# Optimization experiments

Hardware: AMD Instinct MI355X
Metric: run time of the kernel (lower is better)

## Reference

```python
import jax, jax.numpy as jnp
import numpy as np

N_NODES = 100000
N_EDGES = 1600000
IN_CH = 128
HID = 64
N_CLASSES = 16
N_GRAPHS = 64


def setup_inputs() -> dict:
    key = jax.random.key(0)
    ks = jax.random.split(key, 10)
    x = jax.random.normal(ks[0], (N_NODES, IN_CH), dtype=jnp.float32)
    edge_index = jax.random.randint(ks[1], (2, N_EDGES), 0, N_NODES, dtype=jnp.int64)
    edge_weight = jax.random.uniform(ks[2], (N_EDGES,), dtype=jnp.float32)
    batch = jnp.sort(jax.random.randint(ks[3], (N_NODES,), 0, N_GRAPHS, dtype=jnp.int64))
    s1 = 1.0 / np.sqrt(IN_CH)
    s2 = 1.0 / np.sqrt(HID)
    W1 = jax.random.uniform(ks[4], (IN_CH, HID), jnp.float32, -s1, s1)
    b1 = jnp.zeros((HID,), jnp.float32)
    W2 = jax.random.uniform(ks[5], (HID, HID), jnp.float32, -s2, s2)
    b2 = jnp.zeros((HID,), jnp.float32)
    Wl = jax.random.uniform(ks[6], (HID, N_CLASSES), jnp.float32, -s2, s2)
    bl = jax.random.uniform(ks[7], (N_CLASSES,), jnp.float32, -s2, s2)
    return {"x": x, "edge_index": edge_index, "edge_weight": edge_weight,
            "batch": batch, "W1": W1, "b1": b1, "W2": W2, "b2": b2,
            "Wl": Wl, "bl": bl}


def _gcn_conv(x, src, dst, ew, W, b, n_nodes):
    # PyG GCNConv: h = x @ W; symmetric normalization with self-loops;
    # out[dst] += norm * h[src]; out += bias.
    deg = jax.ops.segment_sum(ew, dst, num_segments=n_nodes)
    deg_inv_sqrt = jnp.where(deg > 0, jax.lax.rsqrt(jnp.maximum(deg, 1e-30)), 0.0)
    norm = deg_inv_sqrt[src] * ew * deg_inv_sqrt[dst]  # [E']
    h = x @ W                                          # [N, out]
    msg = h[src] * norm[:, None]                       # [E', out] gather
    out = jax.ops.segment_sum(msg, dst, num_segments=n_nodes)  # scatter-add
    return out + b


def reference(x, edge_index, edge_weight, batch, W1, b1, W2, b2, Wl, bl):
    n = x.shape[0]
    # add self loops once (weight 1.0), shared by both conv layers
    loop = jnp.arange(n, dtype=edge_index.dtype)
    src = jnp.concatenate([edge_index[0], loop])
    dst = jnp.concatenate([edge_index[1], loop])
    ew = jnp.concatenate([edge_weight, jnp.ones((n,), edge_weight.dtype)])

    h = jax.nn.relu(_gcn_conv(x, src, dst, ew, W1, b1, n))
    h = jax.nn.relu(_gcn_conv(h, src, dst, ew, W2, b2, n))

    # global_mean_pool over graphs
    sums = jax.ops.segment_sum(h, batch, num_segments=N_GRAPHS)  # [G, HID]
    cnt = jax.ops.segment_sum(jnp.ones((n,), h.dtype), batch, num_segments=N_GRAPHS)
    pooled = sums / jnp.maximum(cnt, 1.0)[:, None]

    return pooled @ Wl + bl
```

## Files before the change

### kernel.cpp

```cpp
#include <hip/hip_runtime.h>
#include <hip/hip_fp16.h>

#define N_NODES   100000
#define N_EDGES   1600000
#define IN_CH     128
#define HID       64
#define N_CLASSES 16
#define N_GRAPHS  64

#define BK_SH     9
#define BK_NODES  512
#define NB        ((N_NODES + BK_NODES - 1) / BK_NODES)
#define BK_CAP    10240
#define CH_EDGES  4096
#define EPT       16
#define NCH       ((N_EDGES + CH_EDGES - 1) / CH_EDGES)
#define AGG_NPW   2

typedef __attribute__((ext_vector_type(8))) short bf16x8;
typedef __attribute__((ext_vector_type(4))) float f32x4;
typedef __attribute__((ext_vector_type(4))) unsigned u32x4;
typedef __attribute__((ext_vector_type(2))) unsigned u32x2;

__device__ __forceinline__ unsigned short f2bf(float f) {
    unsigned u = __float_as_uint(f);
    u += 0x7fffu + ((u >> 16) & 1u);
    return (unsigned short)(u >> 16);
}
__device__ __forceinline__ f32x4 bf4v(uint2 v) {
    u32x4 u;
    u.x = v.x << 16; u.y = v.x & 0xffff0000u;
    u.z = v.y << 16; u.w = v.y & 0xffff0000u;
    return __builtin_bit_cast(f32x4, u);
}
__device__ __forceinline__ float dec_ew(unsigned v) {
    return __half2float(__ushort_as_half((unsigned short)(v >> 17)));
}

#if __has_builtin(__builtin_amdgcn_make_buffer_rsrc) && \
    __has_builtin(__builtin_amdgcn_raw_buffer_load_b32) && \
    __has_builtin(__builtin_amdgcn_raw_buffer_load_b64)
struct BufView {
    __amdgpu_buffer_rsrc_t rsrc;
    __device__ __forceinline__ void init(const void* p) {
        rsrc = __builtin_amdgcn_make_buffer_rsrc((void*)p, (short)0,
                                                 (int)0xFFFFFFFF, 0x00020000);
    }
    __device__ __forceinline__ unsigned ld32(unsigned off) const {
        return __builtin_amdgcn_raw_buffer_load_b32(rsrc, (int)off, 0, 0);
    }
    __device__ __forceinline__ uint2 ld64(unsigned off) const {
        u32x2 r = __builtin_amdgcn_raw_buffer_load_b64(rsrc, (int)off, 0, 0);
        return make_uint2(r.x, r.y);
    }
};
#else
struct BufView {
    const char* base;
    __device__ __forceinline__ void init(const void* p) { base = (const char*)p; }
    __device__ __forceinline__ unsigned ld32(unsigned off) const {
        return *(const unsigned*)(base + off);
    }
    __device__ __forceinline__ uint2 ld64(unsigned off) const {
        return *(const uint2*)(base + off);
    }
};
#endif

__global__ void k_init(int* __restrict__ bcursor, float* __restrict__ pooled,
                       float* __restrict__ cnt) {
    int i = blockIdx.x * 256 + threadIdx.x;
    if (i < NB) bcursor[i] = i * BK_CAP;
    if (i < N_GRAPHS * HID) pooled[i] = 0.0f;
    if (i < N_GRAPHS) cnt[i] = 0.0f;
}

__global__ void k_binscatter(const int* __restrict__ src, const int* __restrict__ dst,
                             const float* __restrict__ ew, int* __restrict__ bcursor,
                             int2* __restrict__ bedges) {
    __shared__ int  hist[NB];
    __shared__ int  offs[NB];
    __shared__ int  gbase[NB];
    __shared__ int  sc[256];
    __shared__ int2 stage[CH_EDGES];
    __shared__ int  dest[CH_EDGES];
    const int t = threadIdx.x;
    const int base = blockIdx.x * CH_EDGES;
    const int nloc = min(CH_EDGES, N_EDGES - base);

    for (int i = t; i < NB; i += 256) hist[i] = 0;
    __syncthreads();

    int myb[EPT], myr[EPT], myp[EPT]; float myw[EPT];
#pragma unroll
    for (int j = 0; j < EPT; ++j) {
        int i = base + j * 256 + t;
        if (i < N_EDGES) {
            int s = src[i], d = dst[i];
            int b = d >> BK_SH;
            myb[j] = b;
            myr[j] = atomicAdd(&hist[b], 1);
            myp[j] = s | ((d & (BK_NODES - 1)) << 17);
            myw[j] = ew[i];
        } else {
            myb[j] = -1;
        }
    }
    __syncthreads();

    int v = (t < NB) ? hist[t] : 0;
    sc[t] = v;
    __syncthreads();
    for (int off = 1; off < 256; off <<= 1) {
        int a = (t >= off) ? sc[t - off] : 0;
        __syncthreads();
        sc[t] += a;
        __syncthreads();
    }
    if (t < NB) {
        offs[t] = sc[t] - v;
        gbase[t] = (v > 0) ? atomicAdd(&bcursor[t], v) : 0;
    }
    __syncthreads();

#pragma unroll
    for (int j = 0; j < EPT; ++j) {
        if (myb[j] >= 0) {
            int p = offs[myb[j]] + myr[j];
            stage[p] = make_int2(myp[j], __float_as_int(myw[j]));
            dest[p] = gbase[myb[j]] + myr[j];
        }
    }
    __syncthreads();

    for (int i = t; i < nloc; i += 256)
        bedges[dest[i]] = stage[i];
}

__global__ __launch_bounds__(256) void k_build(const int* __restrict__ bcursor,
                                               const int2* __restrict__ bedges,
                                               int2* __restrict__ rowse,
                                               float* __restrict__ dis,
                                               unsigned* __restrict__ csr) {
    __shared__ int2  eds[BK_CAP];
    __shared__ int   cnt[BK_NODES];
    __shared__ float dsum[BK_NODES];
    __shared__ int   cur[BK_NODES];
    __shared__ int   sc[256];
    const int b = blockIdx.x;
    const int t = threadIdx.x;
    const int beg = b * BK_CAP, end = bcursor[b];
    const int n = end - beg;

    for (int i = t; i < BK_NODES; i += 256) { cnt[i] = 0; dsum[i] = 0.0f; }
    __syncthreads();

    for (int i = t; i < n; i += 256) {
        int2 e = bedges[beg + i];
        eds[i] = e;
        int dl = ((unsigned)e.x) >> 17;
        atomicAdd(&cnt[dl], 1);
        atomicAdd(&dsum[dl], __int_as_float(e.y));
    }
    __syncthreads();

    int a0 = cnt[2 * t], a1 = cnt[2 * t + 1];
    int pair = a0 + a1;
    sc[t] = pair;
    __syncthreads();
    for (int off = 1; off < 256; off <<= 1) {
        int a = (t >= off) ? sc[t - off] : 0;
        __syncthreads();
        sc[t] += a;
        __syncthreads();
    }
    int excl = sc[t] - pair;
    cur[2 * t] = excl;
    cur[2 * t + 1] = excl + a0;
    {
        int n0 = b * BK_NODES + 2 * t;
        if (n0 < N_NODES) {
            rowse[n0] = make_int2(beg + excl, beg + excl + a0);
            dis[n0] = rsqrtf(1.0f + dsum[2 * t]);
        }
        int n1 = n0 + 1;
        if (n1 < N_NODES) {
            rowse[n1] = make_int2(beg + excl + a0, beg + excl + a0 + a1);
            dis[n1] = rsqrtf(1.0f + dsum[2 * t + 1]);
        }
    }
    __syncthreads();

    for (int i = t; i < n; i += 256) {
        int2 e = eds[i];
        int dl = ((unsigned)e.x) >> 17;
        int s = e.x & 0x1FFFF;
        unsigned short w16 = __half_as_ushort(__float2half(__int_as_float(e.y)));
        int pos = beg + atomicAdd(&cur[dl], 1);
        csr[pos] = (unsigned)s | ((unsigned)w16 << 17);
    }
}

template <int K, bool INB>
__global__ __launch_bounds__(256) void k_gemm(const float* __restrict__ x,
                                              const unsigned short* __restrict__ xb,
                                              const float* __restrict__ W,
                                              const float* __restrict__ dis,
                                              unsigned short* __restrict__ hb) {
    constexpr int AS = K + 8;
    __shared__ unsigned short wt[64 * AS];
    const int t    = threadIdx.x;
    const int lane = t & 63;
    const int wave = t >> 6;
    const int m    = lane & 15;
    const int quad = lane >> 4;
    const int rowbase = blockIdx.x * 64;

    bf16x8 afrag[K / 32];

    if constexpr (!INB) {
        __shared__ unsigned short a_s[64 * AS];
        constexpr int CPR = K / 8;
        for (int c = t; c < 64 * CPR; c += 256) {
            int row = c / CPR, cc = c % CPR;
            int gr = rowbase + row;
            float4 v0, v1;
            if (gr < N_NODES) {
                v0 = *(const float4*)&x[(long)gr * K + cc * 8];
                v1 = *(const float4*)&x[(long)gr * K + cc * 8 + 4];
            } else {
                v0 = make_float4(0.f, 0.f, 0.f, 0.f); v1 = v0;
            }
            uint4 p;
            p.x = f2bf(v0.x) | ((unsigned)f2bf(v0.y) << 16);
            p.y = f2bf(v0.z) | ((unsigned)f2bf(v0.w) << 16);
            p.z = f2bf(v1.x) | ((unsigned)f2bf(v1.y) << 16);
            p.w = f2bf(v1.z) | ((unsigned)f2bf(v1.w) << 16);
            *(uint4*)&a_s[row * AS + cc * 8] = p;
        }
        for (int idx = t; idx < K * 64; idx += 256) {
            int k = idx >> 6, n = idx & 63;
            wt[n * AS + k] = f2bf(W[idx]);
        }
        __syncthreads();
#pragma unroll
        for (int ks = 0; ks < K / 32; ++ks)
            afrag[ks] = *(const bf16x8*)&a_s[(wave * 16 + m) * AS + ks * 32 + quad * 8];
    } else {
        const int gr = rowbase + wave * 16 + m;
#pragma unroll
        for (int ks = 0; ks < K / 32; ++ks) {
            if (gr < N_NODES)
                afrag[ks] = *(const bf16x8*)&xb[(long)gr * K + ks * 32 + quad * 8];
            else
                afrag[ks] = (bf16x8){0, 0, 0, 0, 0, 0, 0, 0};
        }
        for (int idx = t; idx < K * 64; idx += 256) {
            int k = idx >> 6, n = idx & 63;
            wt[n * AS + k] = f2bf(W[idx]);
        }
        __syncthreads();
    }

    bf16x8 bfrag[4][K / 32];
#pragma unroll
    for (int nt = 0; nt < 4; ++nt)
#pragma unroll
        for (int ks = 0; ks < K / 32; ++ks)
            bfrag[nt][ks] = *(const bf16x8*)&wt[(nt * 16 + m) * AS + ks * 32 + quad * 8];

    f32x4 acc[4];
#pragma unroll
    for (int nt = 0; nt < 4; ++nt) acc[nt] = (f32x4){0.f, 0.f, 0.f, 0.f};

#pragma unroll
    for (int ks = 0; ks < K / 32; ++ks) {
#pragma unroll
        for (int nt = 0; nt < 4; ++nt)
            acc[nt] = __builtin_amdgcn_mfma_f32_16x16x32_bf16(afrag[ks], bfrag[nt][ks],
                                                              acc[nt], 0, 0, 0);
    }

#pragma unroll
    for (int i = 0; i < 4; ++i) {
        int gr = rowbase + wave * 16 + quad * 4 + i;
        if (gr < N_NODES) {
            float dsc = dis[gr];
#pragma unroll
            for (int nt = 0; nt < 4; ++nt)
                hb[(long)gr * HID + nt * 16 + m] = f2bf(dsc * acc[nt][i]);
        }
    }
}

template <bool OB>
__global__ void k_aggregate(const int2* __restrict__ rowse, const unsigned* __restrict__ csr,
                            const uint2* __restrict__ hb, const float* __restrict__ dis,
                            const float* __restrict__ b, float4* __restrict__ out4,
                            uint2* __restrict__ outb) {
    const int tid  = threadIdx.x;
    const int lane = tid & 63;
    const int g    = lane >> 4;
    const int c4   = lane & 15;
    const int nodebase = (blockIdx.x * 4 + (tid >> 6)) * AGG_NPW;
    const float4 bb = ((const float4*)b)[c4];
    const f32x4 bbv = {bb.x, bb.y, bb.z, bb.w};

    if (nodebase >= N_NODES) return;

    BufView vc; vc.init(csr);
    BufView vh; vh.init(hb);
    const unsigned coff = (unsigned)(c4 << 3);

    int2 rs = rowse[nodebase];
    uint2 hsr = hb[nodebase * 16 + c4];

    for (int j = 0; j < AGG_NPW; ++j) {
        const int node = nodebase + j;
        const int2 rs_c = rs;
        const f32x4 hsv = bf4v(hsr);
        if (j + 1 < AGG_NPW) {
            rs  = rowse[node + 1];
            hsr = hb[(node + 1) * 16 + c4];
        }

        f32x4 acc = (g == 0) ? hsv : (f32x4){0.f, 0.f, 0.f, 0.f};

        int p = rs_c.x;
        const int end = rs_c.y;

        unsigned d0, d1, d2, d3;
        if (p + 16 <= end) {
            const unsigned v = (unsigned)((p + g) << 2);
            d0 = vc.ld32(v);      d1 = vc.ld32(v + 16);
            d2 = vc.ld32(v + 32); d3 = vc.ld32(v + 48);
        }
        while (p + 16 <= end) {
            const unsigned e0 = d0, e1 = d1, e2 = d2, e3 = d3;
            const int pn = p + 16;
            if (pn + 16 <= end) {
                const unsigned v = (unsigned)((pn + g) << 2);
                d0 = vc.ld32(v);      d1 = vc.ld32(v + 16);
                d2 = vc.ld32(v + 32); d3 = vc.ld32(v + 48);
            }
            f32x4 v0 = bf4v(vh.ld64(((e0 & 0x1FFFF) << 7) | coff));
            f32x4 v1 = bf4v(vh.ld64(((e1 & 0x1FFFF) << 7) | coff));
            f32x4 v2 = bf4v(vh.ld64(((e2 & 0x1FFFF) << 7) | coff));
            f32x4 v3 = bf4v(vh.ld64(((e3 & 0x1FFFF) << 7) | coff));
            acc += v0 * dec_ew(e0);
            acc += v1 * dec_ew(e1);
            acc += v2 * dec_ew(e2);
            acc += v3 * dec_ew(e3);
            p = pn;
        }
        if (p < end) {
            const int i0 = p + g, i1 = p + 4 + g, i2 = p + 8 + g, i3 = p + 12 + g;
            const int last = end - 1;
            unsigned e0 = vc.ld32((unsigned)(min(i0, last) << 2));
            unsigned e1 = vc.ld32((unsigned)(min(i1, last) << 2));
            unsigned e2 = vc.ld32((unsigned)(min(i2, last) << 2));
            unsigned e3 = vc.ld32((unsigned)(min(i3, last) << 2));
            f32x4 v0 = bf4v(vh.ld64(((e0 & 0x1FFFF) << 7) | coff));
            f32x4 v1 = bf4v(vh.ld64(((e1 & 0x1FFFF) << 7) | coff));
            f32x4 v2 = bf4v(vh.ld64(((e2 & 0x1FFFF) << 7) | coff));
            f32x4 v3 = bf4v(vh.ld64(((e3 & 0x1FFFF) << 7) | coff));
            const float w0 = (i0 < end) ? dec_ew(e0) : 0.0f;
            const float w1 = (i1 < end) ? dec_ew(e1) : 0.0f;
            const float w2 = (i2 < end) ? dec_ew(e2) : 0.0f;
            const float w3 = (i3 < end) ? dec_ew(e3) : 0.0f;
            acc += v0 * w0;
            acc += v1 * w1;
            acc += v2 * w2;
            acc += v3 * w3;
        }

#pragma unroll
        for (int i = 0; i < 4; ++i) {
            float ta = acc[i];
            ta += __shfl_xor(ta, 16);
            ta += __shfl_xor(ta, 32);
            acc[i] = ta;
        }

        if (g == 0) {
            const float dd = dis[node];
            f32x4 o = acc * dd + bbv;
            o.x = fmaxf(o.x, 0.0f); o.y = fmaxf(o.y, 0.0f);
            o.z = fmaxf(o.z, 0.0f); o.w = fmaxf(o.w, 0.0f);
            if constexpr (OB) {
                uint2 pk;
                pk.x = (unsigned)f2bf(o.x) | ((unsigned)f2bf(o.y) << 16);
                pk.y = (unsigned)f2bf(o.z) | ((unsigned)f2bf(o.w) << 16);
                outb[node * 16 + c4] = pk;
            } else {
                *(f32x4*)&out4[node * 16 + c4] = o;
            }
        }
    }
}

#define POOL_NPB 256
__global__ __launch_bounds__(1024) void k_pool(const float* __restrict__ agg,
                                               const int* __restrict__ batch,
                                               float* __restrict__ pooled,
                                               float* __restrict__ cnt) {
    __shared__ float psh[N_GRAPHS * HID];
    __shared__ float csh[N_GRAPHS];
    const int tid = threadIdx.x;
    const int c = tid & 63;
    const int w = tid >> 6;
    const int nodebase = blockIdx.x * POOL_NPB + w * 16;

    for (int i = tid; i < N_GRAPHS * HID; i += 1024) psh[i] = 0.f;
    if (tid < N_GRAPHS) csh[tid] = 0.f;
    __syncthreads();

    int curg = -1; float accv = 0.f, cntacc = 0.f;
    for (int j = 0; j < 16; ++j) {
        int node = nodebase + j;
        if (node >= N_NODES) break;
        int g = batch[node];
        float v = agg[node * HID + c];
        if (g != curg) {
            if (curg >= 0) {
                atomicAdd(&psh[curg * HID + c], accv);
                if (c == 0) atomicAdd(&csh[curg], cntacc);
            }
            curg = g; accv = 0.f; cntacc = 0.f;
        }
        accv += v; cntacc += 1.f;
    }
    if (curg >= 0) {
        atomicAdd(&psh[curg * HID + c], accv);
        if (c == 0) atomicAdd(&csh[curg], cntacc);
    }
    __syncthreads();

    for (int i = tid; i < N_GRAPHS * HID; i += 1024) {
        if (csh[i >> 6] > 0.f) atomicAdd(&pooled[i], psh[i]);
    }
    if (tid < N_GRAPHS && csh[tid] > 0.f) atomicAdd(&cnt[tid], csh[tid]);
}

__global__ void k_out(const float* __restrict__ pooled, const float* __restrict__ cnt,
                      const float* __restrict__ Wl, const float* __restrict__ bl,
                      float* __restrict__ out) {
    int tid = threadIdx.x;
    int g = tid >> 4, k = tid & 15;
    float inv = 1.0f / fmaxf(cnt[g], 1.0f);
    float acc = 0.f;
#pragma unroll
    for (int h = 0; h < HID; ++h) acc += pooled[g * HID + h] * Wl[h * N_CLASSES + k];
    out[g * N_CLASSES + k] = acc * inv + bl[k];
}

extern "C" void kernel_launch(void* const* d_in, const int* in_sizes, int n_in,
                              void* d_out, int out_size, void* d_ws, size_t ws_size,
                              hipStream_t stream) {
    const float* x     = (const float*)d_in[0];
    const int*   ei    = (const int*)d_in[1];
    const float* ew    = (const float*)d_in[2];
    const int*   batch = (const int*)d_in[3];
    const float* W1    = (const float*)d_in[4];
    const float* b1    = (const float*)d_in[5];
    const float* W2    = (const float*)d_in[6];
    const float* b2    = (const float*)d_in[7];
    const float* Wl    = (const float*)d_in[8];
    const float* bl    = (const float*)d_in[9];

    const int* srcv = ei;
    const int* dstv = ei + N_EDGES;

    char* wsb = (char*)d_ws;
    float*          dis    = (float*)wsb;              wsb += 100352 * 4;
    int2*           rowse  = (int2*)wsb;               wsb += 100352 * 8;
    int*            bcursor= (int*)wsb;                wsb += 256 * 4;
    unsigned*       csr    = (unsigned*)wsb;           wsb += (size_t)NB * BK_CAP * 4;
    unsigned short* hb     = (unsigned short*)wsb;     wsb += N_NODES * HID * 2;
    float*          agg    = (float*)wsb;              wsb += N_NODES * HID * 4;
    float*          pooled = (float*)wsb;              wsb += N_GRAPHS * HID * 4;
    float*          cnt    = (float*)wsb;              wsb += N_GRAPHS * 4;
    float*          out    = (float*)d_out;
    int2*           bedges = (int2*)agg;
    unsigned short* hbA    = (unsigned short*)agg;

    k_init<<<16, 256, 0, stream>>>(bcursor, pooled, cnt);
    k_binscatter<<<NCH, 256, 0, stream>>>(srcv, dstv, ew, bcursor, bedges);
    k_build<<<NB, 256, 0, stream>>>(bcursor, bedges, rowse, dis, csr);

    const int agg_blocks = (N_NODES + 4 * AGG_NPW - 1) / (4 * AGG_NPW);

    k_gemm<IN_CH, false><<<(N_NODES + 63) / 64, 256, 0, stream>>>(x, nullptr, W1, dis, hb);
    k_aggregate<true><<<agg_blocks, 256, 0, stream>>>(rowse, csr, (const uint2*)hb,
                                                      dis, b1, nullptr, (uint2*)hbA);
    k_gemm<HID, true><<<(N_NODES + 63) / 64, 256, 0, stream>>>(nullptr, hbA, W2, dis, hb);
    k_aggregate<false><<<agg_blocks, 256, 0, stream>>>(rowse, csr, (const uint2*)hb,
                                                       dis, b2, (float4*)agg, nullptr);

    k_pool<<<(N_NODES + POOL_NPB - 1) / POOL_NPB, 1024, 0, stream>>>(
        agg, batch, pooled, cnt);
    k_out<<<1, N_GRAPHS * N_CLASSES, 0, stream>>>(pooled, cnt, Wl, bl, out);
}
```

Measured before the change: 260.3 us.

## Fuse mean-pool into second aggregation and interleave two nodes' edge streams

The second aggregate kernel now reduces its output rows into per-graph pooled sums in shared memory and atomically adds them to global memory. This removes the fp32 node-feature write, the separate pool kernel and its reread. Graph counts are now computed in the final kernel by binary search over the sorted batch array instead of atomics. The aggregation loop now alternates 16-edge blocks between a wave's two nodes with software-pipelined gathers to overlap latency, at the cost of more registers and branchier control flow.

```diff
diff --git a/kernel.cpp b/kernel.cpp
--- a/kernel.cpp
+++ b/kernel.cpp
@@ -67,12 +67,10 @@
 };
 #endif
 
-__global__ void k_init(int* __restrict__ bcursor, float* __restrict__ pooled,
-                       float* __restrict__ cnt) {
+__global__ void k_init(int* __restrict__ bcursor, float* __restrict__ pooled) {
     int i = blockIdx.x * 256 + threadIdx.x;
     if (i < NB) bcursor[i] = i * BK_CAP;
     if (i < N_GRAPHS * HID) pooled[i] = 0.0f;
-    if (i < N_GRAPHS) cnt[i] = 0.0f;
 }
 
 __global__ void k_binscatter(const int* __restrict__ src, const int* __restrict__ dst,
@@ -293,161 +291,184 @@
     }
 }
 
+#define NEXTBLK(pb_, eb_, jb_, hv_)                                           \
+    do {                                                                      \
+        if (p0 < e0)      { pb_ = p0; eb_ = e0; jb_ = 0; hv_ = true; p0 += 16; } \
+        else if (p1 < e1) { pb_ = p1; eb_ = e1; jb_ = 1; hv_ = true; p1 += 16; } \
+        else              { hv_ = false; }                                    \
+    } while (0)
+
+#define AGG_STEP(pC_, eC_, jC_, c0_, c1_, c2_, c3_, r0_, r1_, r2_, r3_, hC_,  \
+                 n0_, n1_, n2_, n3_, s0_, s1_, s2_, s3_, hN_)                 \
+    do {                                                                      \
+        const float w0_ = (pC_ + g      < eC_) ? dec_ew(c0_) : 0.f;           \
+        const float w1_ = (pC_ + 4 + g  < eC_) ? dec_ew(c1_) : 0.f;           \
+        const float w2_ = (pC_ + 8 + g  < eC_) ? dec_ew(c2_) : 0.f;           \
+        const float w3_ = (pC_ + 12 + g < eC_) ? dec_ew(c3_) : 0.f;           \
+        const int jcur_ = jC_;                                                \
+        if (hN_) {        \
+            s0_ = vh.ld64(((n0_ & 0x1FFFF) << 7) | coff);                     \
+            s1_ = vh.ld64(((n1_ & 0x1FFFF) << 7) | coff);                     \
+            s2_ = vh.ld64(((n2_ & 0x1FFFF) << 7) | coff);                     \
+            s3_ = vh.ld64(((n3_ & 0x1FFFF) << 7) | coff);                     \
+        }                                                                     \
+        NEXTBLK(pC_, eC_, jC_, hC_);    \
+        if (hC_) {                                                            \
+            const int last_ = eC_ - 1;                                        \
+            c0_ = vc.ld32((unsigned)(min(pC_ + g,      last_) << 2));         \
+            c1_ = vc.ld32((unsigned)(min(pC_ + 4 + g,  last_) << 2));         \
+            c2_ = vc.ld32((unsigned)(min(pC_ + 8 + g,  last_) << 2));         \
+            c3_ = vc.ld32((unsigned)(min(pC_ + 12 + g, last_) << 2));         \
+        }                                                                     \
+        f32x4 t_ = bf4v(r0_) * w0_;                                           \
+        t_ += bf4v(r1_) * w1_;                                                \
+        t_ += bf4v(r2_) * w2_;                                                \
+        t_ += bf4v(r3_) * w3_;                                                \
+        if (jcur_ == 0) acc0 += t_; else acc1 += t_;                          \
+    } while (0)
+
 template <bool OB>
-__global__ void k_aggregate(const int2* __restrict__ rowse, const unsigned* __restrict__ csr,
+__global__ __launch_bounds__(256) void k_aggregate(const int2* __restrict__ rowse,
+                            const unsigned* __restrict__ csr,
                             const uint2* __restrict__ hb, const float* __restrict__ dis,
-                            const float* __restrict__ b, float4* __restrict__ out4,
-                            uint2* __restrict__ outb) {
+                            const float* __restrict__ b, const int* __restrict__ batch,
+                            float* __restrict__ pooled, uint2* __restrict__ outb) {
+    __shared__ float psh[4 * AGG_NPW][HID];
     const int tid  = threadIdx.x;
     const int lane = tid & 63;
     const int g    = lane >> 4;
     const int c4   = lane & 15;
-    const int nodebase = (blockIdx.x * 4 + (tid >> 6)) * AGG_NPW;
+    const int wave = tid >> 6;
+    const int node0 = (blockIdx.x * 4 + wave) * AGG_NPW;
     const float4 bb = ((const float4*)b)[c4];
     const f32x4 bbv = {bb.x, bb.y, bb.z, bb.w};
-
-    if (nodebase >= N_NODES) return;
 
     BufView vc; vc.init(csr);
     BufView vh; vh.init(hb);
     const unsigned coff = (unsigned)(c4 << 3);
 
-    int2 rs = rowse[nodebase];
-    uint2 hsr = hb[nodebase * 16 + c4];
-
-    for (int j = 0; j < AGG_NPW; ++j) {
-        const int node = nodebase + j;
-        const int2 rs_c = rs;
-        const f32x4 hsv = bf4v(hsr);
-        if (j + 1 < AGG_NPW) {
-            rs  = rowse[node + 1];
-            hsr = hb[(node + 1) * 16 + c4];
-        }
-
-        f32x4 acc = (g == 0) ? hsv : (f32x4){0.f, 0.f, 0.f, 0.f};
-
-        int p = rs_c.x;
-        const int end = rs_c.y;
-
-        unsigned d0, d1, d2, d3;
-        if (p + 16 <= end) {
-            const unsigned v = (unsigned)((p + g) << 2);
-            d0 = vc.ld32(v);      d1 = vc.ld32(v + 16);
-            d2 = vc.ld32(v + 32); d3 = vc.ld32(v + 48);
-        }
-        while (p + 16 <= end) {
-            const unsigned e0 = d0, e1 = d1, e2 = d2, e3 = d3;
-            const int pn = p + 16;
-            if (pn + 16 <= end) {
-                const unsigned v = (unsigned)((pn + g) << 2);
-                d0 = vc.ld32(v);      d1 = vc.ld32(v + 16);
-                d2 = vc.ld32(v + 32); d3 = vc.ld32(v + 48);
+    const int2 rs0 = rowse[node0];
+    const int2 rs1 = rowse[node0 + 1];
+    const uint2 hs0 = hb[node0 * 16 + c4];
+    const uint2 hs1 = hb[(node0 + 1) * 16 + c4];
+    const float dd0 = dis[node0];
+    const float dd1 = dis[node0 + 1];
+
+    f32x4 acc0 = (g == 0) ? bf4v(hs0) : (f32x4){0.f, 0.f, 0.f, 0.f};
+    f32x4 acc1 = (g == 0) ? bf4v(hs1) : (f32x4){0.f, 0.f, 0.f, 0.f};
+
+    int p0 = rs0.x, e0 = rs0.y, p1 = rs1.x, e1 = rs1.y;
+
+    int pA = 0, eAn = 0, jA = 0; bool hA = false;
+    int pB = 0, eBn = 0, jB = 0; bool hB = false;
+    unsigned cA0 = 0, cA1 = 0, cA2 = 0, cA3 = 0;
+    unsigned cB0 = 0, cB1 = 0, cB2 = 0, cB3 = 0;
+    uint2 rA0 = {0, 0}, rA1 = {0, 0}, rA2 = {0, 0}, rA3 = {0, 0};
+    uint2 rB0 = {0, 0}, rB1 = {0, 0}, rB2 = {0, 0}, rB3 = {0, 0};
+
+    NEXTBLK(pA, eAn, jA, hA);
+    if (hA) {
+        const int last = eAn - 1;
+        cA0 = vc.ld32((unsigned)(min(pA + g,      last) << 2));
+        cA1 = vc.ld32((unsigned)(min(pA + 4 + g,  last) << 2));
+        cA2 = vc.ld32((unsigned)(min(pA + 8 + g,  last) << 2));
+        cA3 = vc.ld32((unsigned)(min(pA + 12 + g, last) << 2));
+        NEXTBLK(pB, eBn, jB, hB);
+        if (hB) {
+            const int lastB = eBn - 1;
+            cB0 = vc.ld32((unsigned)(min(pB + g,      lastB) << 2));
+            cB1 = vc.ld32((unsigned)(min(pB + 4 + g,  lastB) << 2));
+            cB2 = vc.ld32((unsigned)(min(pB + 8 + g,  lastB) << 2));
+            cB3 = vc.ld32((unsigned)(min(pB + 12 + g, lastB) << 2));
+        }
+        rA0 = vh.ld64(((cA0 & 0x1FFFF) << 7) | coff);
+        rA1 = vh.ld64(((cA1 & 0x1FFFF) << 7) | coff);
+        rA2 = vh.ld64(((cA2 & 0x1FFFF) << 7) | coff);
+        rA3 = vh.ld64(((cA3 & 0x1FFFF) << 7) | coff);
+    }
+
+    bool par = false;
+    while (par ? hB : hA) {
+        if (!par) {
+            AGG_STEP(pA, eAn, jA, cA0, cA1, cA2, cA3, rA0, rA1, rA2, rA3, hA,
+                     cB0, cB1, cB2, cB3, rB0, rB1, rB2, rB3, hB);
+        } else {
+            AGG_STEP(pB, eBn, jB, cB0, cB1, cB2, cB3, rB0, rB1, rB2, rB3, hB,
+                     cA0, cA1, cA2, cA3, rA0, rA1, rA2, rA3, hA);
+        }
+        par = !par;
+    }
+
+#pragma unroll
+    for (int i = 0; i < 4; ++i) {
+        float t0 = acc0[i];
+        t0 += __shfl_xor(t0, 16); t0 += __shfl_xor(t0, 32);
+        acc0[i] = t0;
+        float t1 = acc1[i];
+        t1 += __shfl_xor(t1, 16); t1 += __shfl_xor(t1, 32);
+        acc1[i] = t1;
+    }
+
+    if (g == 0) {
+        f32x4 o0 = acc0 * dd0 + bbv;
+        f32x4 o1 = acc1 * dd1 + bbv;
+        o0.x = fmaxf(o0.x, 0.f); o0.y = fmaxf(o0.y, 0.f);
+        o0.z = fmaxf(o0.z, 0.f); o0.w = fmaxf(o0.w, 0.f);
+        o1.x = fmaxf(o1.x, 0.f); o1.y = fmaxf(o1.y, 0.f);
+        o1.z = fmaxf(o1.z, 0.f); o1.w = fmaxf(o1.w, 0.f);
+        if constexpr (OB) {
+            uint2 pk0, pk1;
+            pk0.x = (unsigned)f2bf(o0.x) | ((unsigned)f2bf(o0.y) << 16);
+            pk0.y = (unsigned)f2bf(o0.z) | ((unsigned)f2bf(o0.w) << 16);
+            pk1.x = (unsigned)f2bf(o1.x) | ((unsigned)f2bf(o1.y) << 16);
+            pk1.y = (unsigned)f2bf(o1.z) | ((unsigned)f2bf(o1.w) << 16);
+            outb[node0 * 16 + c4] = pk0;
+            outb[(node0 + 1) * 16 + c4] = pk1;
+        } else {
+            *(f32x4*)&psh[wave * AGG_NPW][c4 * 4] = o0;
+            *(f32x4*)&psh[wave * AGG_NPW + 1][c4 * 4] = o1;
+        }
+    }
+
+    if constexpr (!OB) {
+        __syncthreads();
+        if (tid < HID) {
+            const int nb0 = blockIdx.x * 4 * AGG_NPW;
+            int curg = batch[nb0];
+            float a = 0.f;
+#pragma unroll
+            for (int j = 0; j < 4 * AGG_NPW; ++j) {
+                int bg = batch[nb0 + j];
+                if (bg != curg) {
+                    atomicAdd(&pooled[curg * HID + tid], a);
+                    a = 0.f; curg = bg;
+                }
+                a += psh[j][tid];
             }
-            f32x4 v0 = bf4v(vh.ld64(((e0 & 0x1FFFF) << 7) | coff));
-            f32x4 v1 = bf4v(vh.ld64(((e1 & 0x1FFFF) << 7) | coff));
-            f32x4 v2 = bf4v(vh.ld64(((e2 & 0x1FFFF) << 7) | coff));
-            f32x4 v3 = bf4v(vh.ld64(((e3 & 0x1FFFF) << 7) | coff));
-            acc += v0 * dec_ew(e0);
-            acc += v1 * dec_ew(e1);
-            acc += v2 * dec_ew(e2);
-            acc += v3 * dec_ew(e3);
-            p = pn;
-        }
-        if (p < end) {
-            const int i0 = p + g, i1 = p + 4 + g, i2 = p + 8 + g, i3 = p + 12 + g;
-            const int last = end - 1;
-            unsigned e0 = vc.ld32((unsigned)(min(i0, last) << 2));
-            unsigned e1 = vc.ld32((unsigned)(min(i1, last) << 2));
-            unsigned e2 = vc.ld32((unsigned)(min(i2, last) << 2));
-            unsigned e3 = vc.ld32((unsigned)(min(i3, last) << 2));
-            f32x4 v0 = bf4v(vh.ld64(((e0 & 0x1FFFF) << 7) | coff));
-            f32x4 v1 = bf4v(vh.ld64(((e1 & 0x1FFFF) << 7) | coff));
-            f32x4 v2 = bf4v(vh.ld64(((e2 & 0x1FFFF) << 7) | coff));
-            f32x4 v3 = bf4v(vh.ld64(((e3 & 0x1FFFF) << 7) | coff));
-            const float w0 = (i0 < end) ? dec_ew(e0) : 0.0f;
-            const float w1 = (i1 < end) ? dec_ew(e1) : 0.0f;
-            const float w2 = (i2 < end) ? dec_ew(e2) : 0.0f;
-            const float w3 = (i3 < end) ? dec_ew(e3) : 0.0f;
-            acc += v0 * w0;
-            acc += v1 * w1;
-            acc += v2 * w2;
-            acc += v3 * w3;
-        }
-
-#pragma unroll
-        for (int i = 0; i < 4; ++i) {
-            float ta = acc[i];
-            ta += __shfl_xor(ta, 16);
-            ta += __shfl_xor(ta, 32);
-            acc[i] = ta;
-        }
-
-        if (g == 0) {
-            const float dd = dis[node];
-            f32x4 o = acc * dd + bbv;
-            o.x = fmaxf(o.x, 0.0f); o.y = fmaxf(o.y, 0.0f);
-            o.z = fmaxf(o.z, 0.0f); o.w = fmaxf(o.w, 0.0f);
-            if constexpr (OB) {
-                uint2 pk;
-                pk.x = (unsigned)f2bf(o.x) | ((unsigned)f2bf(o.y) << 16);
-                pk.y = (unsigned)f2bf(o.z) | ((unsigned)f2bf(o.w) << 16);
-                outb[node * 16 + c4] = pk;
-            } else {
-                *(f32x4*)&out4[node * 16 + c4] = o;
-            }
-        }
-    }
-}
-
-#define POOL_NPB 256
-__global__ __launch_bounds__(1024) void k_pool(const float* __restrict__ agg,
-                                               const int* __restrict__ batch,
-                                               float* __restrict__ pooled,
-                                               float* __restrict__ cnt) {
-    __shared__ float psh[N_GRAPHS * HID];
-    __shared__ float csh[N_GRAPHS];
-    const int tid = threadIdx.x;
-    const int c = tid & 63;
-    const int w = tid >> 6;
-    const int nodebase = blockIdx.x * POOL_NPB + w * 16;
-
-    for (int i = tid; i < N_GRAPHS * HID; i += 1024) psh[i] = 0.f;
-    if (tid < N_GRAPHS) csh[tid] = 0.f;
-    __syncthreads();
-
-    int curg = -1; float accv = 0.f, cntacc = 0.f;
-    for (int j = 0; j < 16; ++j) {
-        int node = nodebase + j;
-        if (node >= N_NODES) break;
-        int g = batch[node];
-        float v = agg[node * HID + c];
-        if (g != curg) {
-            if (curg >= 0) {
-                atomicAdd(&psh[curg * HID + c], accv);
-                if (c == 0) atomicAdd(&csh[curg], cntacc);
-            }
-            curg = g; accv = 0.f; cntacc = 0.f;
-        }
-        accv += v; cntacc += 1.f;
-    }
-    if (curg >= 0) {
-        atomicAdd(&psh[curg * HID + c], accv);
-        if (c == 0) atomicAdd(&csh[curg], cntacc);
-    }
-    __syncthreads();
-
-    for (int i = tid; i < N_GRAPHS * HID; i += 1024) {
-        if (csh[i >> 6] > 0.f) atomicAdd(&pooled[i], psh[i]);
-    }
-    if (tid < N_GRAPHS && csh[tid] > 0.f) atomicAdd(&cnt[tid], csh[tid]);
-}
-
-__global__ void k_out(const float* __restrict__ pooled, const float* __restrict__ cnt,
+            atomicAdd(&pooled[curg * HID + tid], a);
+        }
+    }
+}
+
+__global__ __launch_bounds__(1024) void k_out(const float* __restrict__ pooled,
+                      const int* __restrict__ batch,
                       const float* __restrict__ Wl, const float* __restrict__ bl,
                       float* __restrict__ out) {
+    __shared__ int bnd[N_GRAPHS + 1];
     int tid = threadIdx.x;
+    if (tid <= N_GRAPHS) {
+        int target = tid;
+        int lo = 0, hi = N_NODES;
+        while (lo < hi) {
+            int mid = (lo + hi) >> 1;
+            if (batch[mid] < target) lo = mid + 1; else hi = mid;
+        }
+        bnd[tid] = lo;
+    }
+    __syncthreads();
     int g = tid >> 4, k = tid & 15;
-    float inv = 1.0f / fmaxf(cnt[g], 1.0f);
+    float cntg = (float)(bnd[g + 1] - bnd[g]);
+    float inv = 1.0f / fmaxf(cntg, 1.0f);
     float acc = 0.f;
 #pragma unroll
     for (int h = 0; h < HID; ++h) acc += pooled[g * HID + h] * Wl[h * N_CLASSES + k];
@@ -477,14 +498,13 @@
     int*            bcursor= (int*)wsb;                wsb += 256 * 4;
     unsigned*       csr    = (unsigned*)wsb;           wsb += (size_t)NB * BK_CAP * 4;
     unsigned short* hb     = (unsigned short*)wsb;     wsb += N_NODES * HID * 2;
-    float*          agg    = (float*)wsb;              wsb += N_NODES * HID * 4;
+    char*           scratch= wsb;                      wsb += N_NODES * HID * 4;
     float*          pooled = (float*)wsb;              wsb += N_GRAPHS * HID * 4;
-    float*          cnt    = (float*)wsb;              wsb += N_GRAPHS * 4;
     float*          out    = (float*)d_out;
-    int2*           bedges = (int2*)agg;
-    unsigned short* hbA    = (unsigned short*)agg;
-
-    k_init<<<16, 256, 0, stream>>>(bcursor, pooled, cnt);
+    int2*           bedges = (int2*)scratch;
+    unsigned short* hbA    = (unsigned short*)scratch;
+
+    k_init<<<16, 256, 0, stream>>>(bcursor, pooled);
     k_binscatter<<<NCH, 256, 0, stream>>>(srcv, dstv, ew, bcursor, bedges);
     k_build<<<NB, 256, 0, stream>>>(bcursor, bedges, rowse, dis, csr);
 
@@ -492,12 +512,10 @@
 
     k_gemm<IN_CH, false><<<(N_NODES + 63) / 64, 256, 0, stream>>>(x, nullptr, W1, dis, hb);
     k_aggregate<true><<<agg_blocks, 256, 0, stream>>>(rowse, csr, (const uint2*)hb,
-                                                      dis, b1, nullptr, (uint2*)hbA);
+                                                      dis, b1, batch, nullptr, (uint2*)hbA);
     k_gemm<HID, true><<<(N_NODES + 63) / 64, 256, 0, stream>>>(nullptr, hbA, W2, dis, hb);
     k_aggregate<false><<<agg_blocks, 256, 0, stream>>>(rowse, csr, (const uint2*)hb,
-                                                       dis, b2, (float4*)agg, nullptr);
-
-    k_pool<<<(N_NODES + POOL_NPB - 1) / POOL_NPB, 1024, 0, stream>>>(
-        agg, batch, pooled, cnt);
-    k_out<<<1, N_GRAPHS * N_CLASSES, 0, stream>>>(pooled, cnt, Wl, bl, out);
-}
+                                                       dis, b2, batch, pooled, nullptr);
+
+    k_out<<<1, 1024, 0, stream>>>(pooled, batch, Wl, bl, out);
+}
```

Measured after the change: 274.7 us. 1.06x slower.

## Fuse mean-pool into second aggregation and derive graph counts by binary search

Applied to the files above, without the earlier changes.

The second aggregation kernel now keeps its per-node outputs in shared memory. It then reduces them per graph and atomically adds into the pooled sums, which removes the 25.6 MB fp32 agg write, the later read, and the separate pool kernel. Node counts per graph come from a binary search over the sorted batch array inside the output kernel, so the count accumulation goes away. In exchange it adds a block barrier, global atomics per block (one per graph segment per channel), and relies on N_NODES being divisible by 8 and on batch being sorted.

```diff
diff --git a/kernel.cpp b/kernel.cpp
--- a/kernel.cpp
+++ b/kernel.cpp
@@ -67,12 +67,10 @@
 };
 #endif
 
-__global__ void k_init(int* __restrict__ bcursor, float* __restrict__ pooled,
-                       float* __restrict__ cnt) {
+__global__ void k_init(int* __restrict__ bcursor, float* __restrict__ pooled) {
     int i = blockIdx.x * 256 + threadIdx.x;
     if (i < NB) bcursor[i] = i * BK_CAP;
     if (i < N_GRAPHS * HID) pooled[i] = 0.0f;
-    if (i < N_GRAPHS) cnt[i] = 0.0f;
 }
 
 __global__ void k_binscatter(const int* __restrict__ src, const int* __restrict__ dst,
@@ -294,19 +292,20 @@
 }
 
 template <bool OB>
-__global__ void k_aggregate(const int2* __restrict__ rowse, const unsigned* __restrict__ csr,
+__global__ void k_aggregate(const int2* __restrict__ rowse,
+                            const unsigned* __restrict__ csr,
                             const uint2* __restrict__ hb, const float* __restrict__ dis,
-                            const float* __restrict__ b, float4* __restrict__ out4,
-                            uint2* __restrict__ outb) {
+                            const float* __restrict__ b, const int* __restrict__ batch,
+                            float* __restrict__ pooled, uint2* __restrict__ outb) {
+    __shared__ float psh[4 * AGG_NPW][HID];
     const int tid  = threadIdx.x;
     const int lane = tid & 63;
     const int g    = lane >> 4;
     const int c4   = lane & 15;
-    const int nodebase = (blockIdx.x * 4 + (tid >> 6)) * AGG_NPW;
+    const int wave = tid >> 6;
+    const int nodebase = (blockIdx.x * 4 + wave) * AGG_NPW;
     const float4 bb = ((const float4*)b)[c4];
     const f32x4 bbv = {bb.x, bb.y, bb.z, bb.w};
-
-    if (nodebase >= N_NODES) return;
 
     BufView vc; vc.init(csr);
     BufView vh; vh.init(hb);
@@ -393,61 +392,50 @@
                 pk.y = (unsigned)f2bf(o.z) | ((unsigned)f2bf(o.w) << 16);
                 outb[node * 16 + c4] = pk;
             } else {
-                *(f32x4*)&out4[node * 16 + c4] = o;
+                *(f32x4*)&psh[wave * AGG_NPW + j][c4 * 4] = o;
             }
         }
     }
-}
-
-#define POOL_NPB 256
-__global__ __launch_bounds__(1024) void k_pool(const float* __restrict__ agg,
-                                               const int* __restrict__ batch,
-                                               float* __restrict__ pooled,
-                                               float* __restrict__ cnt) {
-    __shared__ float psh[N_GRAPHS * HID];
-    __shared__ float csh[N_GRAPHS];
-    const int tid = threadIdx.x;
-    const int c = tid & 63;
-    const int w = tid >> 6;
-    const int nodebase = blockIdx.x * POOL_NPB + w * 16;
-
-    for (int i = tid; i < N_GRAPHS * HID; i += 1024) psh[i] = 0.f;
-    if (tid < N_GRAPHS) csh[tid] = 0.f;
-    __syncthreads();
-
-    int curg = -1; float accv = 0.f, cntacc = 0.f;
-    for (int j = 0; j < 16; ++j) {
-        int node = nodebase + j;
-        if (node >= N_NODES) break;
-        int g = batch[node];
-        float v = agg[node * HID + c];
-        if (g != curg) {
-            if (curg >= 0) {
-                atomicAdd(&psh[curg * HID + c], accv);
-                if (c == 0) atomicAdd(&csh[curg], cntacc);
+
+    if constexpr (!OB) {
+        __syncthreads();
+        if (tid < HID) {
+            const int nb0 = blockIdx.x * 4 * AGG_NPW;
+            int curg = batch[nb0];
+            float a = 0.f;
+#pragma unroll
+            for (int j = 0; j < 4 * AGG_NPW; ++j) {
+                int bg = batch[nb0 + j];
+                if (bg != curg) {
+                    atomicAdd(&pooled[curg * HID + tid], a);
+                    a = 0.f; curg = bg;
+                }
+                a += psh[j][tid];
             }
-            curg = g; accv = 0.f; cntacc = 0.f;
-        }
-        accv += v; cntacc += 1.f;
-    }
-    if (curg >= 0) {
-        atomicAdd(&psh[curg * HID + c], accv);
-        if (c == 0) atomicAdd(&csh[curg], cntacc);
-    }
-    __syncthreads();
-
-    for (int i = tid; i < N_GRAPHS * HID; i += 1024) {
-        if (csh[i >> 6] > 0.f) atomicAdd(&pooled[i], psh[i]);
-    }
-    if (tid < N_GRAPHS && csh[tid] > 0.f) atomicAdd(&cnt[tid], csh[tid]);
-}
-
-__global__ void k_out(const float* __restrict__ pooled, const float* __restrict__ cnt,
+            atomicAdd(&pooled[curg * HID + tid], a);
+        }
+    }
+}
+
+__global__ __launch_bounds__(1024) void k_out(const float* __restrict__ pooled,
+                      const int* __restrict__ batch,
                       const float* __restrict__ Wl, const float* __restrict__ bl,
                       float* __restrict__ out) {
+    __shared__ int bnd[N_GRAPHS + 1];
     int tid = threadIdx.x;
+    if (tid <= N_GRAPHS) {
+        int target = tid;
+        int lo = 0, hi = N_NODES;
+        while (lo < hi) {
+            int mid = (lo + hi) >> 1;
+            if (batch[mid] < target) lo = mid + 1; else hi = mid;
+        }
+        bnd[tid] = lo;
+    }
+    __syncthreads();
     int g = tid >> 4, k = tid & 15;
-    float inv = 1.0f / fmaxf(cnt[g], 1.0f);
+    float cntg = (float)(bnd[g + 1] - bnd[g]);
+    float inv = 1.0f / fmaxf(cntg, 1.0f);
     float acc = 0.f;
 #pragma unroll
     for (int h = 0; h < HID; ++h) acc += pooled[g * HID + h] * Wl[h * N_CLASSES + k];
@@ -477,27 +465,24 @@
     int*            bcursor= (int*)wsb;                wsb += 256 * 4;
     unsigned*       csr    = (unsigned*)wsb;           wsb += (size_t)NB * BK_CAP * 4;
     unsigned short* hb     = (unsigned short*)wsb;     wsb += N_NODES * HID * 2;
-    float*          agg    = (float*)wsb;              wsb += N_NODES * HID * 4;
+    char*           scratch= wsb;                      wsb += N_NODES * HID * 4;
     float*          pooled = (float*)wsb;              wsb += N_GRAPHS * HID * 4;
-    float*          cnt    = (float*)wsb;              wsb += N_GRAPHS * 4;
     float*          out    = (float*)d_out;
-    int2*           bedges = (int2*)agg;
-    unsigned short* hbA    = (unsigned short*)agg;
-
-    k_init<<<16, 256, 0, stream>>>(bcursor, pooled, cnt);
+    int2*           bedges = (int2*)scratch;
+    unsigned short* hbA    = (unsigned short*)scratch;
+
+    k_init<<<16, 256, 0, stream>>>(bcursor, pooled);
     k_binscatter<<<NCH, 256, 0, stream>>>(srcv, dstv, ew, bcursor, bedges);
     k_build<<<NB, 256, 0, stream>>>(bcursor, bedges, rowse, dis, csr);
 
-    const int agg_blocks = (N_NODES + 4 * AGG_NPW - 1) / (4 * AGG_NPW);
+    const int agg_blocks = N_NODES / (4 * AGG_NPW);
 
     k_gemm<IN_CH, false><<<(N_NODES + 63) / 64, 256, 0, stream>>>(x, nullptr, W1, dis, hb);
     k_aggregate<true><<<agg_blocks, 256, 0, stream>>>(rowse, csr, (const uint2*)hb,
-                                                      dis, b1, nullptr, (uint2*)hbA);
+                                                      dis, b1, batch, nullptr, (uint2*)hbA);
     k_gemm<HID, true><<<(N_NODES + 63) / 64, 256, 0, stream>>>(nullptr, hbA, W2, dis, hb);
     k_aggregate<false><<<agg_blocks, 256, 0, stream>>>(rowse, csr, (const uint2*)hb,
-                                                       dis, b2, (float4*)agg, nullptr);
-
-    k_pool<<<(N_NODES + POOL_NPB - 1) / POOL_NPB, 1024, 0, stream>>>(
-        agg, batch, pooled, cnt);
-    k_out<<<1, N_GRAPHS * N_CLASSES, 0, stream>>>(pooled, cnt, Wl, bl, out);
-}
+                                                       dis, b2, batch, pooled, nullptr);
+
+    k_out<<<1, 1024, 0, stream>>>(pooled, batch, Wl, bl, out);
+}
```

After: 263.9 us. Within noise of the previous version (+1.4%).
